# Kernel tuning notes

Measured on AMD Instinct MI355X. Metric: run time of the kernel, lower is better.

## Reference

```python
import jax, jax.numpy as jnp
import numpy as np

ALPHA = 0.01
EPS = 1e-5


def _lsa(cost):
    """Shortest-augmenting-path linear sum assignment (scipy-style).
    cost: (n, m) float64 with n <= m. Returns col4row: column matched to each row."""
    n, m = cost.shape
    u = np.zeros(n)
    v = np.zeros(m)
    row4col = np.full(m, -1, dtype=np.int64)
    col4row = np.full(n, -1, dtype=np.int64)
    for cur_row in range(n):
        shortest = np.full(m, np.inf)
        path = np.full(m, -1, dtype=np.int64)
        SR = np.zeros(n, dtype=bool)
        SC = np.zeros(m, dtype=bool)
        min_val = 0.0
        i = cur_row
        sink = -1
        while sink == -1:
            SR[i] = True
            idx = np.nonzero(~SC)[0]
            d = min_val + cost[i, idx] - u[i] - v[idx]
            better = d < shortest[idx]
            upd = idx[better]
            shortest[upd] = d[better]
            path[upd] = i
            j = idx[np.argmin(shortest[idx])]
            min_val = shortest[j]
            SC[j] = True
            if row4col[j] == -1:
                sink = j
            else:
                i = row4col[j]
        u[cur_row] += min_val
        sr = SR.copy()
        sr[cur_row] = False
        rows = np.nonzero(sr)[0]
        u[rows] += min_val - shortest[col4row[rows]]
        cols = np.nonzero(SC)[0]
        v[cols] -= min_val - shortest[cols]
        # augment along the path
        j = sink
        while True:
            i = path[j]
            row4col[j] = i
            col4row[i], j = j, col4row[i]
            if i == cur_row:
                break
    return col4row


def hungarian(C):
    """C: (N_pred, M_targ) with N_pred >= M_targ. Returns matched (inp_idx, targ_idx)."""
    col4row = _lsa(C.T)  # rows = targets, cols = preds
    targ_idx = np.arange(C.shape[1])
    inp_idx = col4row
    return inp_idx, targ_idx


def setup_inputs() -> dict:
    key = jax.random.key(0)
    k1, k2 = jax.random.split(key)
    B, N, M = 16, 2048, 256
    pred = jax.random.uniform(k1, (B, N, 5), dtype=jnp.float32)   # coords + confidence in (0,1)
    label = jax.random.uniform(k2, (B, M, 4), dtype=jnp.float32)
    return {"pred": pred, "label": label}


def reference(pred, label):
    # N_pred >= N_targ here so the label truncation branch is a no-op.
    # Original overwrites `loss` each batch iteration (not +=) in the
    # nonempty-label branch, so only the last batch element survives.
    b = pred.shape[0] - 1
    inp = pred[b, :, 0:4]           # [N, 4]
    targ = label[b]                 # [M, 4]
    conf = pred[b, :, 4]            # [N]
    log_c = jnp.log(conf + EPS)
    log_c_anti = jnp.log(1.0 - conf + EPS)

    diff = inp[:, None, :] - targ[None, :, :]          # [N, M, 4]
    normed_diff = jnp.sum(diff * diff, axis=2)         # ||.||_2 ** 2 -> [N, M]
    C = ALPHA * normed_diff - log_c[:, None] + log_c_anti[:, None]

    # Hungarian assignment on host (mirrors .cpu().detach() + scipy in original)
    C_np = np.asarray(jax.device_get(C), dtype=np.float64)
    inp_idx, targ_idx = hungarian(C_np)
    inp_idx = jnp.asarray(inp_idx)
    targ_idx = jnp.asarray(targ_idx)

    matched = jnp.zeros(inp.shape[0], dtype=bool).at[inp_idx].set(True)
    location_loss = ALPHA * jnp.sum(normed_diff[inp_idx, targ_idx])
    confidence_loss = -jnp.sum(log_c[inp_idx]) - jnp.sum(jnp.where(matched, 0.0, log_c_anti))
    return location_loss + confidence_loss
```

## Files before the change

### kernel.cpp

```cpp
#include <hip/hip_runtime.h>
#include <math.h>

#define ALPHA 0.01f
#define EPSF  1e-5f
#define NPRED 2048
#define MTARG 256
#define NT    256
#define CPT   8
#define KMAX  512
#define SPT   2
#define NW    4
#define MARGIN 0.041f
#define BIGF  1e30f
#define EPSA  0.032f
#define MAXROUND 30000
#define IINF 0x7FFFFFFF
#define SLO   (-11.6f)
#define SRANGE 23.3f
#define SBINS 256

__device__ __forceinline__ unsigned int ordf(float v) {
  const unsigned int b = __float_as_uint(v);
  return (v >= 0.0f) ? (b | 0x80000000u) : ~b;
}
__device__ __forceinline__ float unordf(unsigned int u) {
  return __uint_as_float((u & 0x80000000u) ? (u & 0x7FFFFFFFu) : ~u);
}

__launch_bounds__(NT, 1)
__global__ void lap_loss_kernel(const float* __restrict__ pred,
                                const float* __restrict__ label,
                                float* __restrict__ out) {
  __shared__ float4 s_k4[KMAX];
  __shared__ float  s_cc[KMAX];
  __shared__ float  s_cp[KMAX];
  __shared__ short  s_row4col[KMAX];
  __shared__ short  s_argr[KMAX];
  __shared__ int    s_bC[KMAX];
  __shared__ float  s_u[MTARG];
  __shared__ short  s_col4row[MTARG];
  __shared__ float4 s_m2t[MTARG];
  __shared__ float  s_rc[MTARG];
  __shared__ short  s_amin[MTARG];
  __shared__ int    s_bR[MTARG];
  __shared__ int   s_hist[SBINS];
  __shared__ int   s_cnt[CPT * NW];
  __shared__ float s_scr[NW];
  __shared__ float s_pivot, s_sumlca;
  __shared__ int   s_K;

  const int tid  = threadIdx.x;
  const int wave = tid >> 6;
  const int lane = tid & 63;
  const unsigned long long laneLT = (lane == 63) ? 0x7FFFFFFFFFFFFFFFull
                                                 : ((1ull << lane) - 1ull);
  const float* pbase = pred  + (size_t)15 * NPRED * 5;
  const float* lbase = label + (size_t)15 * MTARG * 4;

  s_hist[tid] = 0;
  __syncthreads();

  float mys[CPT];
  float lca_acc = 0.0f;
#pragma unroll
  for (int k = 0; k < CPT; ++k) {
    const int j = tid + k * NT;
    const float c = pbase[j * 5 + 4];
    const float lc  = logf(c + EPSF);
    const float lca = logf(1.0f - c + EPSF);
    mys[k] = lca - lc;
    lca_acc += lca;
    int b = (int)((mys[k] - SLO) * ((float)SBINS / SRANGE));
    b = b < 0 ? 0 : (b > SBINS - 1 ? SBINS - 1 : b);
    atomicAdd(&s_hist[b], 1);
  }
#pragma unroll
  for (int off = 32; off > 0; off >>= 1) lca_acc += __shfl_down(lca_acc, off);
  if (lane == 0) s_scr[wave] = lca_acc;
  __syncthreads();
  if (tid == 0) {
    float s = 0.0f;
    for (int w = 0; w < NW; ++w) s += s_scr[w];
    s_sumlca = s;
  }

  if (tid < 64) {
    const int4 h = *(const int4*)&s_hist[tid * 4];
    const int loc = h.x + h.y + h.z + h.w;
    int scan = loc;
#pragma unroll
    for (int off = 1; off < 64; off <<= 1) {
      const int o = __shfl_up(scan, off);
      if (lane >= off) scan += o;
    }
    int c = scan - loc;
    int cb = IINF;
    c += h.x; if (cb == IINF && c >= MTARG) cb = 4 * tid + 0;
    c += h.y; if (cb == IINF && c >= MTARG) cb = 4 * tid + 1;
    c += h.z; if (cb == IINF && c >= MTARG) cb = 4 * tid + 2;
    c += h.w; if (cb == IINF && c >= MTARG) cb = 4 * tid + 3;
#pragma unroll
    for (int off = 1; off < 64; off <<= 1) {
      const int o = __shfl_xor(cb, off);
      if (o < cb) cb = o;
    }
    if (lane == 0) s_pivot = SLO + (float)(cb + 1) * (SRANGE / (float)SBINS);
  }
  __syncthreads();

  const float keepThr = s_pivot + MARGIN;
  unsigned long long km[CPT];
#pragma unroll
  for (int k = 0; k < CPT; ++k) {
    km[k] = __ballot(mys[k] <= keepThr);
    if (lane == 0) s_cnt[k * NW + wave] = (int)__popcll(km[k]);
  }
#pragma unroll
  for (int k = 0; k < SPT; ++k) s_bC[tid + k * NT] = IINF;
  {
    const float* t = lbase + tid * 4;
    const float tx = t[0], ty = t[1], tz = t[2], tw = t[3];
    s_m2t[tid] = make_float4(-2.0f*ALPHA*tx, -2.0f*ALPHA*ty, -2.0f*ALPHA*tz, -2.0f*ALPHA*tw);
    s_rc[tid]  = ALPHA * (tx*tx + ty*ty + tz*tz + tw*tw);
    s_col4row[tid] = -1;
    s_bR[tid] = IINF;
  }
  __syncthreads();
  {
    int cnts[CPT][NW];
#pragma unroll
    for (int k = 0; k < CPT; ++k)
#pragma unroll
      for (int w = 0; w < NW; ++w) cnts[k][w] = s_cnt[k * NW + w];
    int pre = 0;
    int Ktot = 0;
#pragma unroll
    for (int k = 0; k < CPT; ++k)
#pragma unroll
      for (int w = 0; w < NW; ++w) Ktot += cnts[k][w];
#pragma unroll
    for (int k = 0; k < CPT; ++k) {
      int base = pre;
#pragma unroll
      for (int w = 0; w < NW; ++w) { if (w < wave) base += cnts[k][w]; pre += cnts[k][w]; }
      if (mys[k] <= keepThr) {
        const int slot = base + (int)__popcll(km[k] & laneLT);
        if (slot < KMAX) {
          const int j = tid + k * NT;
          const float* p = pbase + j * 5;
          const float x = p[0], y = p[1], z = p[2], w4 = p[3];
          s_k4[slot] = make_float4(x, y, z, w4);
          s_cc[slot] = ALPHA * (x*x + y*y + z*z + w4*w4) + mys[k];
          s_row4col[slot] = -1;
        }
      }
    }
    if (tid == 0) s_K = Ktot < KMAX ? Ktot : KMAX;
  }
  __syncthreads();
  const int K = s_K;

  {
    const float4 m2 = s_m2t[tid];
    const float  rc = s_rc[tid];
    float best = BIGF; int bj = 0;
    for (int slot = 0; slot < K; ++slot) {
      const float4 q = s_k4[slot];
      const float d = rc + s_cc[slot]
                    + m2.x*q.x + m2.y*q.y + m2.z*q.z + m2.w*q.w;
      if (d < best) { best = d; bj = slot; }
    }
    s_u[tid] = best;
    s_amin[tid] = (short)bj;
  }
  __syncthreads();

#pragma unroll
  for (int k = 0; k < SPT; ++k) {
    const int slot = tid + k * NT;
    if (slot < K) {
      const float4 q = s_k4[slot];
      const float cc = s_cc[slot];
      float best = BIGF; int br = -1;
      for (int i = 0; i < MTARG; ++i) {
        const float4 m2 = s_m2t[i];
        const float d = s_rc[i] + cc - s_u[i]
                      + m2.x*q.x + m2.y*q.y + m2.z*q.z + m2.w*q.w;
        if (d < best) { best = d; br = i; }
      }
      s_cp[slot] = cc - best;
      s_argr[slot] = (short)br;
    } else if (slot < KMAX) {
      s_cp[slot] = BIGF;
      s_argr[slot] = -1;
    }
  }
  __syncthreads();

  atomicMin(&s_bC[(int)s_amin[tid]], tid);
  __syncthreads();
#pragma unroll
  for (int k = 0; k < SPT; ++k) {
    const int j = tid + k * NT;
    if (j < K) {
      const int w = s_bC[j];
      if (w != IINF) { s_row4col[j] = (short)w; s_col4row[w] = (short)j; }
    }
  }
  __syncthreads();
#pragma unroll
  for (int k = 0; k < SPT; ++k) {
    const int j = tid + k * NT;
    if (j < K && s_row4col[j] < 0) {
      const int r = (int)s_argr[j];
      if (r >= 0 && s_col4row[r] < 0) atomicMin(&s_bR[r], j);
    }
  }
  __syncthreads();
  {
    const int j = s_bR[tid];
    if (s_col4row[tid] < 0 && j != IINF) {
      s_col4row[tid] = (short)j;
      s_row4col[j] = (short)tid;
    }
  }
  __syncthreads();

  if (tid < 64) {
    const int l8 = lane & 7;
    const int g  = lane >> 3;
    for (int round = 0; round < MAXROUND; ++round) {
      const unsigned long long m0 = __ballot(s_col4row[lane      ] < 0);
      const unsigned long long m1 = __ballot(s_col4row[lane + 64 ] < 0);
      const unsigned long long m2b= __ballot(s_col4row[lane + 128] < 0);
      const unsigned long long m3 = __ballot(s_col4row[lane + 192] < 0);
      const int c0 = (int)__popcll(m0), c1 = (int)__popcll(m1);
      const int c2 = (int)__popcll(m2b), c3 = (int)__popcll(m3);
      const int U = c0 + c1 + c2 + c3;
      if (U == 0) break;
      const int nb = U < 8 ? U : 8;

      int r = -1;
      if (g < nb) {
        int rem = g; unsigned long long mm; int base;
        if (rem < c0)            { mm = m0;  base = 0; }
        else if (rem < c0+c1)    { mm = m1;  base = 64;  rem -= c0; }
        else if (rem < c0+c1+c2) { mm = m2b; base = 128; rem -= c0 + c1; }
        else                     { mm = m3;  base = 192; rem -= c0 + c1 + c2; }
        int pos = 0;
#pragma unroll
        for (int w = 32; w >= 1; w >>= 1) {
          const unsigned long long msk = ((1ull << w) - 1ull) << pos;
          const int cw = (int)__popcll(mm & msk);
          if (rem >= cw) { rem -= cw; pos += w; }
        }
        r = base + pos;
      }

      int j1 = -1;
      unsigned long long bkey = 0ull;
      if (r >= 0) {
        const float4 mt = s_m2t[r];
        unsigned long long key = ~0ull;
        unsigned int w2u = 0xFFFFFFFFu;
        for (int j = l8; j < K; j += 8) {
          const float4 q4 = s_k4[j];
          const float v = s_cp[j]
                        + mt.x*q4.x + mt.y*q4.y + mt.z*q4.z + mt.w*q4.w;
          const unsigned long long k2 =
              ((unsigned long long)ordf(v) << 32) | (unsigned int)j;
          if (k2 < key) { w2u = (unsigned int)(key >> 32); key = k2; }
          else { const unsigned int o = (unsigned int)(k2 >> 32); if (o < w2u) w2u = o; }
        }
#pragma unroll
        for (int off = 1; off < 8; off <<= 1) {
          const unsigned long long ok = __shfl_xor(key, off);
          const unsigned int ow2 = __shfl_xor(w2u, off);
          if (ok < key) {
            const unsigned int v1 = (unsigned int)(key >> 32);
            w2u = (ow2 < v1) ? ow2 : v1;
            key = ok;
          } else {
            const unsigned int o1 = (unsigned int)(ok >> 32);
            if (o1 < w2u) w2u = o1;
          }
        }
        if (l8 == 0) {
          j1 = (int)(key & 0xFFFFFFFFull);
          const float w1f = unordf((unsigned int)(key >> 32));
          const float w2f = unordf(w2u);
          const float ncp = s_cp[j1] + (w2f - w1f) + EPSA;
          bkey = ((unsigned long long)ordf(ncp) << 32) | (unsigned int)r;
        }
      }

      if (l8 == 0) {
        int J[8]; unsigned long long B[8];
#pragma unroll
        for (int g2 = 0; g2 < 8; ++g2) {
          J[g2] = __shfl(j1, g2 * 8);
          B[g2] = __shfl(bkey, g2 * 8);
        }
        if (j1 >= 0) {
          bool win = true;
#pragma unroll
          for (int g2 = 0; g2 < 8; ++g2)
            if (J[g2] == j1 && B[g2] > bkey) win = false;
          if (win) {
            const int old = (int)s_row4col[j1];
            s_cp[j1] = unordf((unsigned int)(bkey >> 32));
            s_row4col[j1] = (short)r;
            s_col4row[r]  = (short)j1;
            if (old >= 0) s_col4row[old] = -1;
          }
        }
      }
      __threadfence_block();
    }
    if (lane == 0) {
      for (int i = 0; i < MTARG; ++i) {
        if (s_col4row[i] < 0) {
          for (int j = 0; j < K; ++j)
            if (s_row4col[j] < 0) { s_row4col[j] = (short)i; s_col4row[i] = (short)j; break; }
        }
      }
    }
  }
  __syncthreads();

  float acc;
  {
    const int j = (int)s_col4row[tid];
    const float4 q = s_k4[j];
    const float4 m2 = s_m2t[tid];
    acc = s_rc[tid] + s_cc[j]
        + m2.x*q.x + m2.y*q.y + m2.z*q.z + m2.w*q.w;
  }
#pragma unroll
  for (int off = 32; off > 0; off >>= 1) acc += __shfl_down(acc, off);
  __syncthreads();
  if (lane == 0) s_scr[wave] = acc;
  __syncthreads();
  if (tid == 0) {
    float s = 0.0f;
    for (int w = 0; w < NW; ++w) s += s_scr[w];
    out[0] = s - s_sumlca;
  }
}

extern "C" void kernel_launch(void* const* d_in, const int* in_sizes, int n_in,
                              void* d_out, int out_size, void* d_ws, size_t ws_size,
                              hipStream_t stream) {
  const float* pred  = (const float*)d_in[0];
  const float* label = (const float*)d_in[1];
  float* out = (float*)d_out;
  hipLaunchKernelGGL(lap_loss_kernel, dim3(1), dim3(NT), 0, stream,
                     pred, label, out);
}
```

Measured before the change: 199.8 us.

## Adapt auction bidder group width to unassigned count and track masks in registers

```diff
diff --git a/kernel.cpp b/kernel.cpp
--- a/kernel.cpp
+++ b/kernel.cpp
@@ -227,26 +227,29 @@
   __syncthreads();
 
   if (tid < 64) {
-    const int l8 = lane & 7;
-    const int g  = lane >> 3;
+    unsigned long long um0 = __ballot(s_col4row[lane      ] < 0);
+    unsigned long long um1 = __ballot(s_col4row[lane + 64 ] < 0);
+    unsigned long long um2 = __ballot(s_col4row[lane + 128] < 0);
+    unsigned long long um3 = __ballot(s_col4row[lane + 192] < 0);
+
     for (int round = 0; round < MAXROUND; ++round) {
-      const unsigned long long m0 = __ballot(s_col4row[lane      ] < 0);
-      const unsigned long long m1 = __ballot(s_col4row[lane + 64 ] < 0);
-      const unsigned long long m2b= __ballot(s_col4row[lane + 128] < 0);
-      const unsigned long long m3 = __ballot(s_col4row[lane + 192] < 0);
-      const int c0 = (int)__popcll(m0), c1 = (int)__popcll(m1);
-      const int c2 = (int)__popcll(m2b), c3 = (int)__popcll(m3);
+      const int c0 = (int)__popcll(um0), c1 = (int)__popcll(um1);
+      const int c2 = (int)__popcll(um2), c3 = (int)__popcll(um3);
       const int U = c0 + c1 + c2 + c3;
       if (U == 0) break;
       const int nb = U < 8 ? U : 8;
+      const int lg = 31 - __builtin_clz(64 / nb);
+      const int G  = 1 << lg;
+      const int g  = lane >> lg;
+      const int l  = lane & (G - 1);
 
       int r = -1;
       if (g < nb) {
         int rem = g; unsigned long long mm; int base;
-        if (rem < c0)            { mm = m0;  base = 0; }
-        else if (rem < c0+c1)    { mm = m1;  base = 64;  rem -= c0; }
-        else if (rem < c0+c1+c2) { mm = m2b; base = 128; rem -= c0 + c1; }
-        else                     { mm = m3;  base = 192; rem -= c0 + c1 + c2; }
+        if (rem < c0)            { mm = um0; base = 0; }
+        else if (rem < c0+c1)    { mm = um1; base = 64;  rem -= c0; }
+        else if (rem < c0+c1+c2) { mm = um2; base = 128; rem -= c0 + c1; }
+        else                     { mm = um3; base = 192; rem -= c0 + c1 + c2; }
         int pos = 0;
 #pragma unroll
         for (int w = 32; w >= 1; w >>= 1) {
@@ -263,7 +266,7 @@
         const float4 mt = s_m2t[r];
         unsigned long long key = ~0ull;
         unsigned int w2u = 0xFFFFFFFFu;
-        for (int j = l8; j < K; j += 8) {
+        for (int j = l; j < K; j += G) {
           const float4 q4 = s_k4[j];
           const float v = s_cp[j]
                         + mt.x*q4.x + mt.y*q4.y + mt.z*q4.z + mt.w*q4.w;
@@ -272,8 +275,7 @@
           if (k2 < key) { w2u = (unsigned int)(key >> 32); key = k2; }
           else { const unsigned int o = (unsigned int)(k2 >> 32); if (o < w2u) w2u = o; }
         }
-#pragma unroll
-        for (int off = 1; off < 8; off <<= 1) {
+        for (int off = 1; off < G; off <<= 1) {
           const unsigned long long ok = __shfl_xor(key, off);
           const unsigned int ow2 = __shfl_xor(w2u, off);
           if (ok < key) {
@@ -285,33 +287,69 @@
             if (o1 < w2u) w2u = o1;
           }
         }
-        if (l8 == 0) {
+        if (l == 0) {
           j1 = (int)(key & 0xFFFFFFFFull);
-          const float w1f = unordf((unsigned int)(key >> 32));
-          const float w2f = unordf(w2u);
-          const float ncp = s_cp[j1] + (w2f - w1f) + EPSA;
+          const float ncp = s_cp[j1]
+                          + (unordf(w2u) - unordf((unsigned int)(key >> 32))) + EPSA;
           bkey = ((unsigned long long)ordf(ncp) << 32) | (unsigned int)r;
         }
       }
 
-      if (l8 == 0) {
-        int J[8]; unsigned long long B[8];
-#pragma unroll
-        for (int g2 = 0; g2 < 8; ++g2) {
-          J[g2] = __shfl(j1, g2 * 8);
-          B[g2] = __shfl(bkey, g2 * 8);
-        }
-        if (j1 >= 0) {
-          bool win = true;
-#pragma unroll
-          for (int g2 = 0; g2 < 8; ++g2)
-            if (J[g2] == j1 && B[g2] > bkey) win = false;
-          if (win) {
-            const int old = (int)s_row4col[j1];
-            s_cp[j1] = unordf((unsigned int)(bkey >> 32));
-            s_row4col[j1] = (short)r;
-            s_col4row[r]  = (short)j1;
-            if (old >= 0) s_col4row[old] = -1;
+      int Jv[8]; unsigned long long Bv[8]; int Rv[8];
+#pragma unroll
+      for (int g2 = 0; g2 < 8; ++g2) {
+        const int src = (g2 << lg) & 63;
+        Jv[g2] = __shfl(j1, src);
+        Bv[g2] = __shfl(bkey, src);
+        Rv[g2] = __shfl(r, src);
+        if (g2 >= nb) { Jv[g2] = -1; Bv[g2] = 0ull; Rv[g2] = -1; }
+      }
+
+      bool win[8];
+#pragma unroll
+      for (int g2 = 0; g2 < 8; ++g2) {
+        bool w = (Jv[g2] >= 0);
+#pragma unroll
+        for (int g3 = 0; g3 < 8; ++g3)
+          if (g3 != g2 && Jv[g3] == Jv[g2] && Bv[g3] > Bv[g2]) w = false;
+        win[g2] = w;
+      }
+
+      bool mywin = false; int myJ = -1, myR = -1;
+      unsigned long long myB = 0ull;
+#pragma unroll
+      for (int g2 = 0; g2 < 8; ++g2)
+        if (lane == g2) { mywin = win[g2]; myJ = Jv[g2]; myR = Rv[g2]; myB = Bv[g2]; }
+
+      int oldv = -1;
+      if (mywin && myJ >= 0) oldv = (int)s_row4col[myJ];
+      int Ov[8];
+#pragma unroll
+      for (int g2 = 0; g2 < 8; ++g2) Ov[g2] = __shfl(oldv, g2);
+
+      if (mywin && myJ >= 0) {
+        s_cp[myJ] = unordf((unsigned int)(myB >> 32));
+        s_row4col[myJ] = (short)myR;
+        s_col4row[myR] = (short)myJ;
+        if (oldv >= 0) s_col4row[oldv] = -1;
+      }
+
+#pragma unroll
+      for (int g2 = 0; g2 < 8; ++g2) {
+        if (win[g2] && Jv[g2] >= 0) {
+          const int rr = Rv[g2];
+          const unsigned long long rb = 1ull << (rr & 63);
+          if (rr < 64)       um0 &= ~rb;
+          else if (rr < 128) um1 &= ~rb;
+          else if (rr < 192) um2 &= ~rb;
+          else               um3 &= ~rb;
+          const int oo = Ov[g2];
+          if (oo >= 0) {
+            const unsigned long long ob = 1ull << (oo & 63);
+            if (oo < 64)       um0 |= ob;
+            else if (oo < 128) um1 |= ob;
+            else if (oo < 192) um2 |= ob;
+            else               um3 |= ob;
           }
         }
       }
```

After: 301.5 us. +50.9%, slower.

## Add epsilon-scaling two-phase auction and float-based top-2 search

Applied to the files above, without the earlier changes.

```diff
diff --git a/kernel.cpp b/kernel.cpp
--- a/kernel.cpp
+++ b/kernel.cpp
@@ -9,10 +9,12 @@
 #define CPT   8
 #define KMAX  512
 #define SPT   2
+#define SPL   8
 #define NW    4
 #define MARGIN 0.041f
 #define BIGF  1e30f
-#define EPSA  0.032f
+#define EPSA1 0.25f
+#define EPSA2 0.032f
 #define MAXROUND 30000
 #define IINF 0x7FFFFFFF
 #define SLO   (-11.6f)
@@ -229,93 +231,96 @@
   if (tid < 64) {
     const int l8 = lane & 7;
     const int g  = lane >> 3;
-    for (int round = 0; round < MAXROUND; ++round) {
-      const unsigned long long m0 = __ballot(s_col4row[lane      ] < 0);
-      const unsigned long long m1 = __ballot(s_col4row[lane + 64 ] < 0);
-      const unsigned long long m2b= __ballot(s_col4row[lane + 128] < 0);
-      const unsigned long long m3 = __ballot(s_col4row[lane + 192] < 0);
-      const int c0 = (int)__popcll(m0), c1 = (int)__popcll(m1);
-      const int c2 = (int)__popcll(m2b), c3 = (int)__popcll(m3);
-      const int U = c0 + c1 + c2 + c3;
-      if (U == 0) break;
-      const int nb = U < 8 ? U : 8;
-
-      int r = -1;
-      if (g < nb) {
-        int rem = g; unsigned long long mm; int base;
-        if (rem < c0)            { mm = m0;  base = 0; }
-        else if (rem < c0+c1)    { mm = m1;  base = 64;  rem -= c0; }
-        else if (rem < c0+c1+c2) { mm = m2b; base = 128; rem -= c0 + c1; }
-        else                     { mm = m3;  base = 192; rem -= c0 + c1 + c2; }
-        int pos = 0;
-#pragma unroll
-        for (int w = 32; w >= 1; w >>= 1) {
-          const unsigned long long msk = ((1ull << w) - 1ull) << pos;
-          const int cw = (int)__popcll(mm & msk);
-          if (rem >= cw) { rem -= cw; pos += w; }
-        }
-        r = base + pos;
-      }
-
-      int j1 = -1;
-      unsigned long long bkey = 0ull;
-      if (r >= 0) {
-        const float4 mt = s_m2t[r];
-        unsigned long long key = ~0ull;
-        unsigned int w2u = 0xFFFFFFFFu;
-        for (int j = l8; j < K; j += 8) {
-          const float4 q4 = s_k4[j];
-          const float v = s_cp[j]
-                        + mt.x*q4.x + mt.y*q4.y + mt.z*q4.z + mt.w*q4.w;
-          const unsigned long long k2 =
-              ((unsigned long long)ordf(v) << 32) | (unsigned int)j;
-          if (k2 < key) { w2u = (unsigned int)(key >> 32); key = k2; }
-          else { const unsigned int o = (unsigned int)(k2 >> 32); if (o < w2u) w2u = o; }
-        }
-#pragma unroll
-        for (int off = 1; off < 8; off <<= 1) {
-          const unsigned long long ok = __shfl_xor(key, off);
-          const unsigned int ow2 = __shfl_xor(w2u, off);
-          if (ok < key) {
-            const unsigned int v1 = (unsigned int)(key >> 32);
-            w2u = (ow2 < v1) ? ow2 : v1;
-            key = ok;
-          } else {
-            const unsigned int o1 = (unsigned int)(ok >> 32);
-            if (o1 < w2u) w2u = o1;
-          }
-        }
+    for (int ph = 0; ph < 2; ++ph) {
+      const float eps = ph ? EPSA2 : EPSA1;
+      if (ph) {
+#pragma unroll
+        for (int q = 0; q < 4; ++q) s_col4row[lane + 64 * q] = -1;
+#pragma unroll
+        for (int k = 0; k < SPL; ++k) s_row4col[lane + 64 * k] = -1;
+        __threadfence_block();
+      }
+      for (int round = 0; round < MAXROUND; ++round) {
+        const unsigned long long m0 = __ballot(s_col4row[lane      ] < 0);
+        const unsigned long long m1 = __ballot(s_col4row[lane + 64 ] < 0);
+        const unsigned long long m2b= __ballot(s_col4row[lane + 128] < 0);
+        const unsigned long long m3 = __ballot(s_col4row[lane + 192] < 0);
+        const int c0 = (int)__popcll(m0), c1 = (int)__popcll(m1);
+        const int c2 = (int)__popcll(m2b), c3 = (int)__popcll(m3);
+        const int U = c0 + c1 + c2 + c3;
+        if (U == 0) break;
+        const int nb = U < 8 ? U : 8;
+
+        int r = -1;
+        if (g < nb) {
+          int rem = g; unsigned long long mm; int base;
+          if (rem < c0)            { mm = m0;  base = 0; }
+          else if (rem < c0+c1)    { mm = m1;  base = 64;  rem -= c0; }
+          else if (rem < c0+c1+c2) { mm = m2b; base = 128; rem -= c0 + c1; }
+          else                     { mm = m3;  base = 192; rem -= c0 + c1 + c2; }
+          int pos = 0;
+#pragma unroll
+          for (int w = 32; w >= 1; w >>= 1) {
+            const unsigned long long msk = ((1ull << w) - 1ull) << pos;
+            const int cw = (int)__popcll(mm & msk);
+            if (rem >= cw) { rem -= cw; pos += w; }
+          }
+          r = base + pos;
+        }
+
+        int j1 = -1;
+        unsigned long long bkey = 0ull;
+        if (r >= 0) {
+          const float4 mt = s_m2t[r];
+          float w1 = BIGF, w2 = BIGF; int jb = 0x7FFFFFFF;
+          for (int j = l8; j < K; j += 8) {
+            const float4 q4 = s_k4[j];
+            const float v = s_cp[j]
+                          + mt.x*q4.x + mt.y*q4.y + mt.z*q4.z + mt.w*q4.w;
+            if (v < w1) { w2 = w1; w1 = v; jb = j; }
+            else if (v < w2) { w2 = v; }
+          }
+#pragma unroll
+          for (int off = 1; off < 8; off <<= 1) {
+            const float ow1 = __shfl_xor(w1, off);
+            const float ow2 = __shfl_xor(w2, off);
+            const int   ojb = __shfl_xor(jb, off);
+            if (ow1 < w1 || (ow1 == w1 && ojb < jb)) {
+              w2 = fminf(w1, ow2); w1 = ow1; jb = ojb;
+            } else {
+              w2 = fminf(w2, ow1);
+            }
+          }
+          if (l8 == 0) {
+            j1 = jb;
+            const float ncp = s_cp[j1] + (w2 - w1) + eps;
+            bkey = ((unsigned long long)ordf(ncp) << 32) | (unsigned int)r;
+          }
+        }
+
         if (l8 == 0) {
-          j1 = (int)(key & 0xFFFFFFFFull);
-          const float w1f = unordf((unsigned int)(key >> 32));
-          const float w2f = unordf(w2u);
-          const float ncp = s_cp[j1] + (w2f - w1f) + EPSA;
-          bkey = ((unsigned long long)ordf(ncp) << 32) | (unsigned int)r;
-        }
-      }
-
-      if (l8 == 0) {
-        int J[8]; unsigned long long B[8];
-#pragma unroll
-        for (int g2 = 0; g2 < 8; ++g2) {
-          J[g2] = __shfl(j1, g2 * 8);
-          B[g2] = __shfl(bkey, g2 * 8);
-        }
-        if (j1 >= 0) {
-          bool win = true;
-#pragma unroll
-          for (int g2 = 0; g2 < 8; ++g2)
-            if (J[g2] == j1 && B[g2] > bkey) win = false;
-          if (win) {
-            const int old = (int)s_row4col[j1];
-            s_cp[j1] = unordf((unsigned int)(bkey >> 32));
-            s_row4col[j1] = (short)r;
-            s_col4row[r]  = (short)j1;
-            if (old >= 0) s_col4row[old] = -1;
-          }
-        }
-      }
-      __threadfence_block();
+          int J[8]; unsigned long long B[8];
+#pragma unroll
+          for (int g2 = 0; g2 < 8; ++g2) {
+            J[g2] = __shfl(j1, g2 * 8);
+            B[g2] = __shfl(bkey, g2 * 8);
+          }
+          if (j1 >= 0) {
+            bool win = true;
+#pragma unroll
+            for (int g2 = 0; g2 < 8; ++g2)
+              if (J[g2] == j1 && B[g2] > bkey) win = false;
+            if (win) {
+              const int old = (int)s_row4col[j1];
+              s_cp[j1] = unordf((unsigned int)(bkey >> 32));
+              s_row4col[j1] = (short)r;
+              s_col4row[r]  = (short)j1;
+              if (old >= 0) s_col4row[old] = -1;
+            }
+          }
+        }
+        __threadfence_block();
+      }
     }
     if (lane == 0) {
       for (int i = 0; i < MTARG; ++i) {
```

Result: slower. 596.9 us (+198.8%).
